# Kernel optimization log

Measured on AMD Instinct MI355X. Metric: run time of the kernel, lower is better.

Reference implementation:

```python
import jax, jax.numpy as jnp
import numpy as np

B, N, P, D, NH, DFFN = 4, 1024, 128, 512, 8, 2048
DH = D // NH  # 64


def setup_inputs() -> dict:
    key = jax.random.key(0)
    ks = jax.random.split(key, 64)
    i = [0]
    def rn(shape, s=1.0):
        k = ks[i[0]]; i[0] += 1
        return jax.random.normal(k, shape, jnp.float32) * s
    w = 0.05  # weight init scale
    inp = {
        "H": rn((B, N, D)),
        "V": rn((B, N, 3, D)),
        "D_batch": rn((B, N, N)),
        "rbf_bias": rn((B, 1, N, N)),  # rbf_feat_batch[layer_idx]
        "prompt_feature": rn((B * P, D)),
        # self-attn params
        "Wq": rn((4 * D, D), w), "bq": jnp.zeros((4 * D,), jnp.float32),
        "Wk": rn((4 * D, D), w), "bk": jnp.zeros((4 * D,), jnp.float32),
        "Wv": rn((D, D), w), "bv": jnp.zeros((D,), jnp.float32),
        "Wvv": rn((D, D), w),
        "Wo": rn((D, D), w), "bo": jnp.zeros((D,), jnp.float32),
        "Wvo": rn((D, D), w),
        "ln1_g": jnp.ones((D,), jnp.float32), "ln1_b": jnp.zeros((D,), jnp.float32),
        # cross-attn params (nn.MultiheadAttention packed in_proj + out_proj, then scaler_o)
        "ca_in_w": rn((3 * D, D), w), "ca_in_b": jnp.zeros((3 * D,), jnp.float32),
        "ca_out_w": rn((D, D), w), "ca_out_b": jnp.zeros((D,), jnp.float32),
        "ca_so_w": rn((D, D), w), "ca_so_b": jnp.zeros((D,), jnp.float32),
        "ln2_g": jnp.ones((D,), jnp.float32), "ln2_b": jnp.zeros((D,), jnp.float32),
        # GVP-FFN params
        "ffn_lv": rn((2 * D, D), w),
        "ffn_w1": rn((DFFN, 2 * D), w), "ffn_b1": jnp.zeros((DFFN,), jnp.float32),
        "ffn_w2": rn((2 * D, DFFN), w), "ffn_b2": jnp.zeros((2 * D,), jnp.float32),
        "ln3_g": jnp.ones((D,), jnp.float32), "ln3_b": jnp.zeros((D,), jnp.float32),
        # key-validity mask [B,N]
        "H_mask": jax.random.randint(ks[60], (B, N), 0, 2).astype(jnp.int32),
    }
    return inp


def _ln(x, g, b):
    m = x.mean(-1, keepdims=True)
    v = ((x - m) ** 2).mean(-1, keepdims=True)
    return (x - m) / jnp.sqrt(v + 1e-5) * g + b


def _ept_layer(H, V, D_batch, rbf_bias, prompt_feature,
               Wq, bq, Wk, bk, Wv, bv, Wvv, Wo, bo, Wvo, ln1_g, ln1_b,
               ca_in_w, ca_in_b, ca_out_w, ca_out_b, ca_so_w, ca_so_b, ln2_g, ln2_b,
               ffn_lv, ffn_w1, ffn_b1, ffn_w2, ffn_b2, ln3_g, ln3_b, H_mask):
    factor = 0.5 / np.sqrt(DH)
    # ---- self-attn sublayer (pre-LN on H, residual on H and V) ----
    H0, V0 = H, V
    Hn = _ln(H, ln1_g, ln1_b)
    Hq = (Hn @ Wq.T + bq).reshape(B, N, NH, 4 * DH)
    Hk = (Hn @ Wk.T + bk).reshape(B, N, NH, 4 * DH)
    Hv = (Hn @ Wv.T + bv).reshape(B, N, NH, DH)
    # vector values: [B,N,3,D] -> [B,N,3,NH,DH] -> [B,N,NH,3,DH] -> [B,N,NH,3*DH]
    Vv = (V @ Wvv.T).reshape(B, N, 3, NH, DH).transpose(0, 1, 3, 2, 4).reshape(B, N, NH, 3 * DH)
    V_attn = jnp.concatenate([Hv, Vv], axis=-1)  # [B,N,NH,4*DH]
    bias = rbf_bias + D_batch[:, None]           # [B,1,N,N]
    bias = jnp.where(H_mask[:, None, None, :] == 0, -jnp.inf, bias)
    scores = jnp.einsum('bnhd,bmhd->bhnm', Hq, Hk) * factor + bias
    attn = jax.nn.softmax(scores, axis=-1)
    res = jnp.einsum('bhnm,bmhd->bnhd', attn, V_attn)  # [B,N,NH,4*DH]
    H_res = res[..., :DH].reshape(B, N, D)
    V_res = res[..., DH:].reshape(B, N, NH, 3, DH).transpose(0, 1, 3, 2, 4).reshape(B, N, 3, D)
    H = (H_res @ Wo.T + bo) + H0
    V = (V_res @ Wvo.T) + V0
    # ---- cross-attn sublayer (pre-LN, residual on H only) ----
    H0 = H
    Hn = _ln(H, ln2_g, ln2_b)
    prompt = prompt_feature.reshape(B, P, D)
    Wq_c, Wk_c, Wv_c = ca_in_w[:D], ca_in_w[D:2 * D], ca_in_w[2 * D:]
    bq_c, bk_c, bv_c = ca_in_b[:D], ca_in_b[D:2 * D], ca_in_b[2 * D:]
    q = (Hn @ Wq_c.T + bq_c).reshape(B, N, NH, DH)
    k = (prompt @ Wk_c.T + bk_c).reshape(B, P, NH, DH)
    v = (prompt @ Wv_c.T + bv_c).reshape(B, P, NH, DH)
    ca = jax.nn.softmax(jnp.einsum('bnhd,bphd->bhnp', q, k) / np.sqrt(DH), axis=-1)
    co = jnp.einsum('bhnp,bphd->bnhd', ca, v).reshape(B, N, D)
    co = co @ ca_out_w.T + ca_out_b
    H = (co @ ca_so_w.T + ca_so_b) + H0
    # ---- GVP-FFN sublayer (pre-LN on H, residual on H and V) ----
    H0, V0 = H, V
    Hn = _ln(H, ln3_g, ln3_b)
    Vp = V @ ffn_lv.T                  # [B,N,3,2D]
    V1, V2 = Vp[..., :D], Vp[..., D:]
    scaler = jnp.concatenate([Hn, jnp.linalg.norm(V1, axis=-2)], axis=-1)  # [B,N,2D]
    h1 = jax.nn.silu(scaler @ ffn_w1.T + ffn_b1)
    so = h1 @ ffn_w2.T + ffn_b2        # [B,N,2D]
    H_out, V_upd = so[..., :D], so[..., D:]
    H = H_out + H0
    V = V_upd[..., None, :] * V2 + V0  # vector_act == 'none'
    return H, V


def reference(H, V, D_batch, rbf_bias, prompt_feature,
              Wq, bq, Wk, bk, Wv, bv, Wvv, Wo, bo, Wvo, ln1_g, ln1_b,
              ca_in_w, ca_in_b, ca_out_w, ca_out_b, ca_so_w, ca_so_b, ln2_g, ln2_b,
              ffn_lv, ffn_w1, ffn_b1, ffn_w2, ffn_b2, ln3_g, ln3_b, H_mask):
    return _ept_layer(H, V, D_batch, rbf_bias, prompt_feature,
                      Wq, bq, Wk, bk, Wv, bv, Wvv, Wo, bo, Wvo, ln1_g, ln1_b,
                      ca_in_w, ca_in_b, ca_out_w, ca_out_b, ca_so_w, ca_so_b, ln2_g, ln2_b,
                      ffn_lv, ffn_w1, ffn_b1, ffn_w2, ffn_b2, ln3_g, ln3_b, H_mask)
```

## Files before the change

kernel.cpp:

```cpp
#include <hip/hip_runtime.h>
#include <cstdint>
#include <cstddef>

#define B_    4
#define N_    1024
#define P_    128
#define D_    512
#define NH_   8

typedef unsigned short ushort_t;
typedef short short8 __attribute__((ext_vector_type(8)));
typedef float f32x4 __attribute__((ext_vector_type(4)));
typedef ushort_t ushort4_t __attribute__((ext_vector_type(4)));

__device__ inline ushort_t f2bf(float f) {
  union { float fp; unsigned int u; } v; v.fp = f;
  unsigned int r = v.u + 0x7fffu + ((v.u >> 16) & 1u);
  return (ushort_t)(r >> 16);
}
__device__ inline float bf2f(ushort_t u) {
  union { unsigned int i; float f; } v; v.i = ((unsigned int)u) << 16;
  return v.f;
}

__device__ __forceinline__ void gll16(const ushort_t* g, ushort_t* l) {
  __builtin_amdgcn_global_load_lds(
      (const __attribute__((address_space(1))) void*)g,
      (__attribute__((address_space(3))) void*)l, 16, 0, 0);
}

__device__ inline void cast8(const float* __restrict__ s, ushort_t* __restrict__ d,
                             unsigned i) {
  const float* sp = s + (size_t)i * 8;
  short8 o;
#pragma unroll
  for (int j = 0; j < 8; ++j) o[j] = (short)f2bf(sp[j]);
  *(short8*)(d + (size_t)i * 8) = o;
}

__global__ __launch_bounds__(256) void cast_fused(
    const float* s0, ushort_t* d0,  const float* s1, ushort_t* d1,
    const float* s2, ushort_t* d2,  const float* s3, ushort_t* d3,
    const float* s4, ushort_t* d4,  const float* s5, ushort_t* d5,
    const float* s6, ushort_t* d6,  const float* s7, ushort_t* d7,
    const float* s8, ushort_t* d8,  const float* s9, ushort_t* d9,
    const float* s10, ushort_t* d10, const float* s11, ushort_t* d11,
    const float* s12, ushort_t* d12, const float* s13, ushort_t* d13)
{
  unsigned i = blockIdx.x * 256 + threadIdx.x;
#define SEG(s, d, n8) if (i < (n8)) { cast8(s, d, i); return; } i -= (n8);
  SEG(s0, d0, 131072u)
  SEG(s1, d1, 131072u)
  SEG(s2, d2, 32768u)
  SEG(s3, d3, 32768u)
  SEG(s4, d4, 32768u)
  SEG(s5, d5, 32768u)
  SEG(s6, d6, 98304u)
  SEG(s7, d7, 32768u)
  SEG(s8, d8, 32768u)
  SEG(s9, d9, 65536u)
  SEG(s10, d10, 262144u)
  SEG(s11, d11, 262144u)
  SEG(s12, d12, 32768u)
  SEG(s13, d13, 786432u)
#undef SEG
}

__global__ __launch_bounds__(256) void biasmerge(const float* __restrict__ bq,
                                                 const float* __restrict__ bk,
                                                 float* __restrict__ o)
{
  int i = blockIdx.x * 256 + threadIdx.x;
  o[i] = (i < 2048) ? bq[i] : bk[i - 2048];
}

__global__ __launch_bounds__(256) void biascomb(const float* __restrict__ Db,
                                                const float* __restrict__ rbf,
                                                const int* __restrict__ mask,
                                                ushort_t* __restrict__ out)
{
  size_t i = (size_t)blockIdx.x * 256 + threadIdx.x;
  size_t e = i * 4;
  int b  = (int)(e >> 20);
  int m0 = (int)(e & 1023);
  float4 r = *(const float4*)(rbf + e);
  float4 d = *(const float4*)(Db + e);
  const int* mp = mask + b * 1024 + m0;
  ushort4_t o;
  o.x = f2bf(mp[0] ? r.x + d.x : -1e30f);
  o.y = f2bf(mp[1] ? r.y + d.y : -1e30f);
  o.z = f2bf(mp[2] ? r.z + d.z : -1e30f);
  o.w = f2bf(mp[3] ? r.w + d.w : -1e30f);
  *(ushort4_t*)(out + e) = o;
}

__global__ __launch_bounds__(256) void ln_kernel(
    const float* __restrict__ x, const float* __restrict__ g,
    const float* __restrict__ bb, ushort_t* __restrict__ y, int ostride)
{
  int row = blockIdx.x;
  int t = threadIdx.x;
  const float* xr = x + (size_t)row * D_;
  float a = xr[t], c = xr[t + 256];
  float s = a + c, sq = a * a + c * c;
#pragma unroll
  for (int off = 32; off >= 1; off >>= 1) {
    s  += __shfl_xor(s, off);
    sq += __shfl_xor(sq, off);
  }
  __shared__ float red[8];
  int w = t >> 6, lane = t & 63;
  if (lane == 0) { red[w] = s; red[4 + w] = sq; }
  __syncthreads();
  float st  = red[0] + red[1] + red[2] + red[3];
  float sqt = red[4] + red[5] + red[6] + red[7];
  float mean = st * (1.0f / D_);
  float var  = sqt * (1.0f / D_) - mean * mean;
  float inv  = rsqrtf(var + 1e-5f);
  y[(size_t)row * ostride + t]       = f2bf((a - mean) * inv * g[t] + bb[t]);
  y[(size_t)row * ostride + t + 256] = f2bf((c - mean) * inv * g[t + 256] + bb[t + 256]);
}

__global__ __launch_bounds__(256) void gemm_bf16(
    const ushort_t* __restrict__ A, const ushort_t* __restrict__ W,
    const float* __restrict__ bias, const float* __restrict__ res,
    float* __restrict__ Cf, ushort_t* __restrict__ Cb,
    int M, int N, int K, int flags)
{
  __shared__ __align__(16) ushort_t Al[128 * 32];
  __shared__ __align__(16) ushort_t Wl[128 * 32];
  const int t = threadIdx.x;
  const int wv = t >> 6, lane = t & 63, lr = lane & 15, lk = lane >> 4;
  const int wr = wv >> 1, wc = wv & 1;
  const size_t row0 = (size_t)blockIdx.y * 128;
  const size_t col0 = (size_t)blockIdx.x * 128;

  const int srow = 32 * wv + (lane >> 2);
  const int scol = (((lane & 3) ^ ((lane >> 3) & 3))) * 8;
  const ushort_t* ApG = A + (row0 + srow) * (size_t)K + scol;
  const ushort_t* WpG = W + (col0 + srow) * (size_t)K + scol;
  ushort_t* AlD = Al + (size_t)(32 * wv) * 32;
  ushort_t* WlD = Wl + (size_t)(32 * wv) * 32;
  const size_t K16 = (size_t)16 * K;

  f32x4 acc[4][4];
#pragma unroll
  for (int i = 0; i < 4; ++i)
#pragma unroll
    for (int j = 0; j < 4; ++j) acc[i][j] = f32x4{0.f, 0.f, 0.f, 0.f};

  const int sx = (lr >> 1) & 3;

  for (int k0 = 0; k0 < K; k0 += 32) {
    __syncthreads();
    gll16(ApG + k0,       AlD);
    gll16(ApG + k0 + K16, AlD + 512);
    gll16(WpG + k0,       WlD);
    gll16(WpG + k0 + K16, WlD + 512);
    __syncthreads();
    short8 af[4], bf[4];
#pragma unroll
    for (int i = 0; i < 4; ++i)
      af[i] = *(const short8*)&Al[(wr * 64 + i * 16 + lr) * 32 + ((lk ^ sx) << 3)];
#pragma unroll
    for (int j = 0; j < 4; ++j)
      bf[j] = *(const short8*)&Wl[(wc * 64 + j * 16 + lr) * 32 + ((lk ^ sx) << 3)];
#pragma unroll
    for (int i = 0; i < 4; ++i)
#pragma unroll
      for (int j = 0; j < 4; ++j)
        acc[i][j] = __builtin_amdgcn_mfma_f32_16x16x32_bf16(af[i], bf[j], acc[i][j], 0, 0, 0);
  }

  const int orow = wr * 64 + lk * 4, ocol = wc * 64 + lr;
#pragma unroll
  for (int i = 0; i < 4; ++i) {
#pragma unroll
    for (int j = 0; j < 4; ++j) {
      size_t colb = col0 + ocol + j * 16;
      float bv = (flags & 1) ? bias[colb] : 0.f;
#pragma unroll
      for (int r = 0; r < 4; ++r) {
        size_t rowg = row0 + orow + i * 16 + r;
        float v = acc[i][j][r] + bv;
        if (flags & 4) v = v / (1.f + __expf(-v));
        if (flags & 2) v += res[rowg * N + colb];
        if (flags & 8)  Cf[rowg * N + colb] = v;
        if (flags & 16) Cb[rowg * N + colb] = f2bf(v);
      }
    }
  }
}

__global__ __launch_bounds__(256) void vt_build(
    const ushort_t* __restrict__ HVb, const ushort_t* __restrict__ VVTb,
    ushort_t* __restrict__ VT)
{
  const int bh = blockIdx.z, b = bh >> 3, h = bh & 7;
  const int n0 = blockIdx.x * 64, dt = blockIdx.y;
  __shared__ __align__(16) ushort_t tile[64][72];
  const int t = threadIdx.x;
  {
    int r = t >> 2, c0 = (t & 3) * 16;
    const ushort_t* src = (dt == 0)
      ? HVb + ((size_t)(b * 1024 + n0 + r)) * 512 + h * 64 + c0
      : VVTb + (((size_t)(b * 1024 + n0 + r)) * 3 + (dt - 1)) * 512 + h * 64 + c0;
    *(short8*)&tile[r][c0]     = *(const short8*)src;
    *(short8*)&tile[r][c0 + 8] = *(const short8*)(src + 8);
  }
  __syncthreads();
  {
    int d = t >> 2, nc = (t & 3) * 16;
    short8 o0, o1;
#pragma unroll
    for (int i = 0; i < 8; ++i) { o0[i] = tile[nc + i][d]; o1[i] = tile[nc + 8 + i][d]; }
    ushort_t* dst = VT + ((size_t)bh * 256 + dt * 64 + d) * 1024 + n0 + nc;
    *(short8*)dst = o0;
    *(short8*)(dst + 8) = o1;
  }
}

__global__ __launch_bounds__(256) void attn_mfma(
    const ushort_t* __restrict__ QKg, const ushort_t* __restrict__ VTg,
    const ushort_t* __restrict__ biasb,
    ushort_t* __restrict__ HRESb, ushort_t* __restrict__ VRESb)
{
  const int bh = blockIdx.y, b = bh >> 3, h = bh & 7;
  const int q0 = blockIdx.x * 64;
  const int t = threadIdx.x, w = t >> 6, lane = t & 63, lr = lane & 15, lk = lane >> 4;

  __shared__ __align__(16) ushort_t Kl[32][264];
  __shared__ __align__(16) ushort_t Vl[256][40];
  __shared__ __align__(16) ushort_t Pl[4][16][40];

  short8 qf[8];
  {
    const ushort_t* qb = QKg + ((size_t)(b * 1024 + q0 + w * 16 + lr)) * 4096 + h * 256;
#pragma unroll
    for (int s = 0; s < 8; ++s) qf[s] = *(const short8*)(qb + s * 32 + lk * 8);
  }
  f32x4 o[16];
#pragma unroll
  for (int i = 0; i < 16; ++i) o[i] = f32x4{0.f, 0.f, 0.f, 0.f};
  float mrow[4] = {-1e30f, -1e30f, -1e30f, -1e30f};
  float lsum[4] = {0.f, 0.f, 0.f, 0.f};
  const int qrow = q0 + w * 16 + lk * 4;

  const int krow = t >> 3, kc = (t & 7) * 32;
  const ushort_t* ksrc = QKg + ((size_t)(b * 1024 + krow)) * 4096 + 2048 + h * 256 + kc;
  const ushort_t* vsrc = VTg + ((size_t)bh * 256 + t) * 1024;
  const int vrot = (t >> 3) & 3;

  for (int k0 = 0; k0 < 1024; k0 += 32) {
    __syncthreads();
    {
      const ushort_t* ks = ksrc + (size_t)k0 * 4096;
#pragma unroll
      for (int c = 0; c < 4; ++c)
        *(short8*)&Kl[krow][kc + c * 8] = *(const short8*)(ks + c * 8);
#pragma unroll
      for (int c = 0; c < 4; ++c) {
        int cc = (c + vrot) & 3;
        *(short8*)&Vl[t][cc * 8] = *(const short8*)(vsrc + k0 + cc * 8);
      }
    }
    __syncthreads();

    f32x4 s2[2];
    s2[0] = f32x4{0.f, 0.f, 0.f, 0.f};
    s2[1] = f32x4{0.f, 0.f, 0.f, 0.f};
    __builtin_amdgcn_s_setprio(1);
#pragma unroll
    for (int ks = 0; ks < 8; ++ks) {
#pragma unroll
      for (int j = 0; j < 2; ++j) {
        short8 kf = *(const short8*)&Kl[j * 16 + lr][ks * 32 + lk * 8];
        s2[j] = __builtin_amdgcn_mfma_f32_16x16x32_bf16(qf[ks], kf, s2[j], 0, 0, 0);
      }
    }
    __builtin_amdgcn_s_setprio(0);

    float sv[2][4];
    const ushort_t* bp = biasb + ((size_t)b << 20) + (size_t)qrow * 1024 + k0 + lr;
#pragma unroll
    for (int r = 0; r < 4; ++r) {
      sv[0][r] = s2[0][r] * 0.0625f + bf2f(bp[r * 1024]);
      sv[1][r] = s2[1][r] * 0.0625f + bf2f(bp[r * 1024 + 16]);
    }
    float pm[4], need = -1e30f;
#pragma unroll
    for (int r = 0; r < 4; ++r) {
      float m2 = fmaxf(sv[0][r], sv[1][r]);
      m2 = fmaxf(m2, __shfl_xor(m2, 1));
      m2 = fmaxf(m2, __shfl_xor(m2, 2));
      m2 = fmaxf(m2, __shfl_xor(m2, 4));
      m2 = fmaxf(m2, __shfl_xor(m2, 8));
      pm[r] = m2;
      need = fmaxf(need, m2 - mrow[r]);
    }
    if (!__all(need <= 8.f)) {
#pragma unroll
      for (int r = 0; r < 4; ++r) {
        float mn = fmaxf(mrow[r], pm[r]);
        float al = __expf(mrow[r] - mn);
        mrow[r] = mn;
        lsum[r] *= al;
#pragma unroll
        for (int d = 0; d < 16; ++d) o[d][r] *= al;
      }
    }
#pragma unroll
    for (int r = 0; r < 4; ++r) {
      float p0 = __expf(sv[0][r] - mrow[r]);
      float p1 = __expf(sv[1][r] - mrow[r]);
      float rs = p0 + p1;
      rs += __shfl_xor(rs, 1); rs += __shfl_xor(rs, 2);
      rs += __shfl_xor(rs, 4); rs += __shfl_xor(rs, 8);
      lsum[r] += rs;
      Pl[w][lk * 4 + r][lr]      = f2bf(p0);
      Pl[w][lk * 4 + r][16 + lr] = f2bf(p1);
    }
    short8 pf = *(const short8*)&Pl[w][lr][lk * 8];
    __builtin_amdgcn_s_setprio(1);
#pragma unroll
    for (int d = 0; d < 16; ++d) {
      short8 vf = *(const short8*)&Vl[d * 16 + lr][lk * 8];
      o[d] = __builtin_amdgcn_mfma_f32_16x16x32_bf16(pf, vf, o[d], 0, 0, 0);
    }
    __builtin_amdgcn_s_setprio(0);
  }

  float inv[4];
#pragma unroll
  for (int r = 0; r < 4; ++r) inv[r] = 1.f / lsum[r];
#pragma unroll
  for (int d = 0; d < 16; ++d) {
    int dcat = d * 16 + lr;
#pragma unroll
    for (int r = 0; r < 4; ++r) {
      float v = o[d][r] * inv[r];
      int n = qrow + r;
      if (dcat < 64)
        HRESb[((size_t)b * 1024 + n) * 512 + h * 64 + dcat] = f2bf(v);
      else {
        int c = (dcat - 64) >> 6, jj = (dcat - 64) & 63;
        VRESb[(((size_t)b * 1024 + n) * 3 + c) * 512 + h * 64 + jj] = f2bf(v);
      }
    }
  }
}

__global__ __launch_bounds__(256) void attn_cross_mfma(
    const ushort_t* __restrict__ Qb, const ushort_t* __restrict__ KVb,
    ushort_t* __restrict__ COb)
{
  const int bh = blockIdx.y, b = bh >> 3, h = bh & 7;
  const int q0 = blockIdx.x * 64;
  const int t = threadIdx.x, w = t >> 6, lane = t & 63, lr = lane & 15, lk = lane >> 4;

  __shared__ __align__(16) ushort_t Kl[128][72];
  __shared__ __align__(16) ushort_t Vt[64][136];
  __shared__ __align__(16) ushort_t Pl[4][16][136];

  {
    int p = t >> 1, c0 = (t & 1) * 32;
    const ushort_t* kp = KVb + ((size_t)b * 128 + p) * 1024 + h * 64 + c0;
#pragma unroll
    for (int i = 0; i < 4; ++i) {
      short8 kv = *(const short8*)(kp + i * 8);
      *(short8*)&Kl[p][c0 + i * 8] = kv;
      short8 vv = *(const short8*)(kp + 512 + i * 8);
#pragma unroll
      for (int jj = 0; jj < 8; ++jj) Vt[c0 + i * 8 + jj][p] = (ushort_t)vv[jj];
    }
  }
  __syncthreads();

  short8 qf[2];
  {
    const ushort_t* qp = Qb + ((size_t)b * 1024 + q0 + w * 16 + lr) * 512 + h * 64;
    qf[0] = *(const short8*)(qp + lk * 8);
    qf[1] = *(const short8*)(qp + 32 + lk * 8);
  }

  f32x4 s[8];
#pragma unroll
  for (int j = 0; j < 8; ++j) s[j] = f32x4{0.f, 0.f, 0.f, 0.f};
#pragma unroll
  for (int ks = 0; ks < 2; ++ks)
#pragma unroll
    for (int j = 0; j < 8; ++j) {
      short8 kf = *(const short8*)&Kl[j * 16 + lr][ks * 32 + lk * 8];
      s[j] = __builtin_amdgcn_mfma_f32_16x16x32_bf16(qf[ks], kf, s[j], 0, 0, 0);
    }

  float linv[4];
#pragma unroll
  for (int r = 0; r < 4; ++r) {
    float sc[8];
#pragma unroll
    for (int j = 0; j < 8; ++j) sc[j] = s[j][r] * 0.125f;
    float mx = sc[0];
#pragma unroll
    for (int j = 1; j < 8; ++j) mx = fmaxf(mx, sc[j]);
    mx = fmaxf(mx, __shfl_xor(mx, 1));
    mx = fmaxf(mx, __shfl_xor(mx, 2));
    mx = fmaxf(mx, __shfl_xor(mx, 4));
    mx = fmaxf(mx, __shfl_xor(mx, 8));
    float rs = 0.f;
#pragma unroll
    for (int j = 0; j < 8; ++j) {
      float p = __expf(sc[j] - mx);
      rs += p;
      Pl[w][lk * 4 + r][j * 16 + lr] = f2bf(p);
    }
    rs += __shfl_xor(rs, 1); rs += __shfl_xor(rs, 2);
    rs += __shfl_xor(rs, 4); rs += __shfl_xor(rs, 8);
    linv[r] = 1.f / rs;
  }
  __syncthreads();

  f32x4 o[4];
#pragma unroll
  for (int d = 0; d < 4; ++d) o[d] = f32x4{0.f, 0.f, 0.f, 0.f};
#pragma unroll
  for (int ks = 0; ks < 4; ++ks) {
    short8 pf = *(const short8*)&Pl[w][lr][ks * 32 + lk * 8];
#pragma unroll
    for (int d = 0; d < 4; ++d) {
      short8 vf = *(const short8*)&Vt[d * 16 + lr][ks * 32 + lk * 8];
      o[d] = __builtin_amdgcn_mfma_f32_16x16x32_bf16(pf, vf, o[d], 0, 0, 0);
    }
  }

#pragma unroll
  for (int d = 0; d < 4; ++d)
#pragma unroll
    for (int r = 0; r < 4; ++r) {
      int n = q0 + w * 16 + lk * 4 + r;
      COb[((size_t)b * 1024 + n) * 512 + h * 64 + d * 16 + lr] = f2bf(o[d][r] * linv[r]);
    }
}

__global__ __launch_bounds__(256) void vnorm_kernel(
    const ushort_t* __restrict__ Vp, ushort_t* __restrict__ scal)
{
  size_t i = (size_t)blockIdx.x * 256 + threadIdx.x;
  size_t bn = i >> 9; int d = (int)(i & 511);
  size_t base = bn * 3 * 1024 + d;
  float a = bf2f(Vp[base]);
  float b = bf2f(Vp[base + 1024]);
  float c = bf2f(Vp[base + 2048]);
  scal[bn * 1024 + 512 + d] = f2bf(sqrtf(a * a + b * b + c * c));
}

__global__ __launch_bounds__(256) void final_kernel(
    const float* __restrict__ so, const float* __restrict__ H2,
    const ushort_t* __restrict__ Vp, const float* __restrict__ Vnew,
    float* __restrict__ out)
{
  size_t i = (size_t)blockIdx.x * 256 + threadIdx.x;
  size_t bn = i >> 9; int d = (int)(i & 511);
  out[bn * 512 + d] = so[bn * 1024 + d] + H2[bn * 512 + d];
  float vu = so[bn * 1024 + 512 + d];
  float* outV = out + (size_t)B_ * N_ * D_;
#pragma unroll
  for (int c = 0; c < 3; ++c) {
    size_t vi = (bn * 3 + c) * 512 + d;
    outV[vi] = vu * bf2f(Vp[(bn * 3 + c) * 1024 + 512 + d]) + Vnew[vi];
  }
}

extern "C" void kernel_launch(void* const* d_in, const int* in_sizes, int n_in,
                              void* d_out, int out_size, void* d_ws, size_t ws_size,
                              hipStream_t stream)
{
  const float* H      = (const float*)d_in[0];
  const float* V      = (const float*)d_in[1];
  const float* Db     = (const float*)d_in[2];
  const float* rbf    = (const float*)d_in[3];
  const float* prompt = (const float*)d_in[4];
  const float* Wq  = (const float*)d_in[5];
  const float* bq  = (const float*)d_in[6];
  const float* Wk  = (const float*)d_in[7];
  const float* bk  = (const float*)d_in[8];
  const float* Wv  = (const float*)d_in[9];
  const float* bv  = (const float*)d_in[10];
  const float* Wvv = (const float*)d_in[11];
  const float* Wo  = (const float*)d_in[12];
  const float* bo  = (const float*)d_in[13];
  const float* Wvo = (const float*)d_in[14];
  const float* ln1g = (const float*)d_in[15];
  const float* ln1b = (const float*)d_in[16];
  const float* caw  = (const float*)d_in[17];
  const float* cab  = (const float*)d_in[18];
  const float* caow = (const float*)d_in[19];
  const float* caob = (const float*)d_in[20];
  const float* casw = (const float*)d_in[21];
  const float* casb = (const float*)d_in[22];
  const float* ln2g = (const float*)d_in[23];
  const float* ln2b = (const float*)d_in[24];
  const float* flv  = (const float*)d_in[25];
  const float* fw1  = (const float*)d_in[26];
  const float* fb1  = (const float*)d_in[27];
  const float* fw2  = (const float*)d_in[28];
  const float* fb2  = (const float*)d_in[29];
  const float* ln3g = (const float*)d_in[30];
  const float* ln3b = (const float*)d_in[31];
  const int*   mask = (const int*)d_in[32];

  char* wsb = (char*)d_ws;
  float* out = (float*)d_out;

#define HMB(x) ((size_t)(x) << 19)
  ushort_t* Wqkb  = (ushort_t*)(wsb + HMB(0));
  ushort_t* Wvb   = (ushort_t*)(wsb + HMB(8));
  ushort_t* Wvvb  = (ushort_t*)(wsb + HMB(9));
  ushort_t* Wob   = (ushort_t*)(wsb + HMB(10));
  ushort_t* Wvob  = (ushort_t*)(wsb + HMB(11));
  ushort_t* cawb  = (ushort_t*)(wsb + HMB(12));
  ushort_t* caowb = (ushort_t*)(wsb + HMB(15));
  ushort_t* caswb = (ushort_t*)(wsb + HMB(16));
  ushort_t* flvb  = (ushort_t*)(wsb + HMB(17));
  ushort_t* fw1b  = (ushort_t*)(wsb + HMB(19));
  ushort_t* fw2b  = (ushort_t*)(wsb + HMB(27));
  ushort_t* promptb = (ushort_t*)(wsb + HMB(35));
  float*    BQK   = (float*)   (wsb + HMB(36));
  ushort_t* HQKb  = (ushort_t*)(wsb + HMB(37));
  float*    VNEW  = (float*)   (wsb + HMB(37));
  float*    H2    = (float*)   (wsb + HMB(85));
  ushort_t* HNb   = (ushort_t*)(wsb + HMB(101));
  ushort_t* VT    = (ushort_t*)(wsb + HMB(101));
  ushort_t* QCb   = (ushort_t*)(wsb + HMB(101));
  ushort_t* KVCb  = (ushort_t*)(wsb + HMB(109));
  ushort_t* SCALb = (ushort_t*)(wsb + HMB(101));
  ushort_t* Vb    = (ushort_t*)(wsb + HMB(133));
  ushort_t* HRESb = (ushort_t*)(wsb + HMB(133));
  ushort_t* HN2b  = (ushort_t*)(wsb + HMB(133));
  ushort_t* VPb   = (ushort_t*)(wsb + HMB(133));
  ushort_t* VRESb = (ushort_t*)(wsb + HMB(141));
  ushort_t* COb   = (ushort_t*)(wsb + HMB(141));
  ushort_t* CO2b  = (ushort_t*)(wsb + HMB(149));
  ushort_t* HVb   = (ushort_t*)(wsb + HMB(157));
  ushort_t* VVTb  = (ushort_t*)(wsb + HMB(165));
  float*    H1    = (float*)   (wsb + HMB(165));
  ushort_t* BIASCb= (ushort_t*)(wsb + HMB(189));
  float*    SO    = (float*)   (wsb + HMB(189));
  ushort_t* VNEWb = (ushort_t*)(wsb + HMB(221));
  ushort_t* HH1b  = (ushort_t*)(wsb + HMB(245));

  cast_fused<<<7680, 256, 0, stream>>>(
      Wq, Wqkb, Wk, Wqkb + (size_t)2048 * 512, Wv, Wvb, Wvv, Wvvb, Wo, Wob,
      Wvo, Wvob, caw, cawb, caow, caowb, casw, caswb, flv, flvb,
      fw1, fw1b, fw2, fw2b, prompt, promptb, V, Vb);
  biasmerge<<<16, 256, 0, stream>>>(bq, bk, BQK);
  biascomb<<<4096, 256, 0, stream>>>(Db, rbf, mask, BIASCb);
  ln_kernel<<<4096, 256, 0, stream>>>(H, ln1g, ln1b, HNb, 512);

  gemm_bf16<<<dim3(32, 32), 256, 0, stream>>>(HNb, Wqkb, BQK, nullptr, nullptr, HQKb, 4096, 4096, 512, 1 | 16);
  gemm_bf16<<<dim3(4, 32), 256, 0, stream>>>(HNb, Wvb, bv, nullptr, nullptr, HVb, 4096, 512, 512, 1 | 16);
  gemm_bf16<<<dim3(4, 96), 256, 0, stream>>>(Vb, Wvvb, nullptr, nullptr, nullptr, VVTb, 12288, 512, 512, 16);

  vt_build<<<dim3(16, 4, 32), 256, 0, stream>>>(HVb, VVTb, VT);

  attn_mfma<<<dim3(16, 32), 256, 0, stream>>>(HQKb, VT, BIASCb, HRESb, VRESb);

  gemm_bf16<<<dim3(4, 32), 256, 0, stream>>>(HRESb, Wob, bo, H, H1, nullptr, 4096, 512, 512, 1 | 2 | 8);
  gemm_bf16<<<dim3(4, 96), 256, 0, stream>>>(VRESb, Wvob, nullptr, V, VNEW, VNEWb, 12288, 512, 512, 2 | 8 | 16);

  ln_kernel<<<4096, 256, 0, stream>>>(H1, ln2g, ln2b, HN2b, 512);
  gemm_bf16<<<dim3(4, 32), 256, 0, stream>>>(HN2b, cawb, cab, nullptr, nullptr, QCb, 4096, 512, 512, 1 | 16);
  gemm_bf16<<<dim3(8, 4), 256, 0, stream>>>(promptb, cawb + 262144, cab + 512, nullptr, nullptr, KVCb, 512, 1024, 512, 1 | 16);

  attn_cross_mfma<<<dim3(16, 32), 256, 0, stream>>>(QCb, KVCb, COb);

  gemm_bf16<<<dim3(4, 32), 256, 0, stream>>>(COb, caowb, caob, nullptr, nullptr, CO2b, 4096, 512, 512, 1 | 16);
  gemm_bf16<<<dim3(4, 32), 256, 0, stream>>>(CO2b, caswb, casb, H1, H2, nullptr, 4096, 512, 512, 1 | 2 | 8);

  gemm_bf16<<<dim3(8, 96), 256, 0, stream>>>(VNEWb, flvb, nullptr, nullptr, nullptr, VPb, 12288, 1024, 512, 16);
  ln_kernel<<<4096, 256, 0, stream>>>(H2, ln3g, ln3b, SCALb, 1024);
  vnorm_kernel<<<8192, 256, 0, stream>>>(VPb, SCALb);

  gemm_bf16<<<dim3(16, 32), 256, 0, stream>>>(SCALb, fw1b, fb1, nullptr, nullptr, HH1b, 4096, 2048, 1024, 1 | 4 | 16);
  gemm_bf16<<<dim3(8, 32), 256, 0, stream>>>(HH1b, fw2b, fb2, nullptr, SO, nullptr, 4096, 1024, 2048, 1 | 8);

  final_kernel<<<8192, 256, 0, stream>>>(SO, H2, VPb, VNEW, out);

  (void)in_sizes; (void)n_in; (void)out_size; (void)ws_size;
}
```

Measured before the change: 550.3 us.

## Prefetch K/V tiles into registers, swizzle K LDS, remap blocks per XCD

The attention kernel now loads the next K and V tile into registers while the current tile is being computed, hiding global-load latency behind the MFMA work. The K shared-memory tile drops its padding and uses an XOR swizzle to avoid bank conflicts. Both the GEMM and attention kernels remap their block indices so that blocks sharing data land on the same XCD, improving L2 reuse on the chiplet layout. The trade-off is higher register pressure from the prefetch buffers, and the remap assumes the block count divides by 8.

```diff
diff --git a/kernel.cpp b/kernel.cpp
--- a/kernel.cpp
+++ b/kernel.cpp
@@ -132,8 +132,13 @@
   const int t = threadIdx.x;
   const int wv = t >> 6, lane = t & 63, lr = lane & 15, lk = lane >> 4;
   const int wr = wv >> 1, wc = wv & 1;
-  const size_t row0 = (size_t)blockIdx.y * 128;
-  const size_t col0 = (size_t)blockIdx.x * 128;
+
+  const int gx = gridDim.x;
+  const int lid = blockIdx.y * gx + blockIdx.x;
+  const int cpx = (gx * gridDim.y) >> 3;
+  const int nlid = (lid & 7) * cpx + (lid >> 3);
+  const size_t row0 = (size_t)(nlid / gx) * 128;
+  const size_t col0 = (size_t)(nlid % gx) * 128;
 
   const int srow = 32 * wv + (lane >> 2);
   const int scol = (((lane & 3) ^ ((lane >> 3) & 3))) * 8;
@@ -225,11 +230,13 @@
     const ushort_t* __restrict__ biasb,
     ushort_t* __restrict__ HRESb, ushort_t* __restrict__ VRESb)
 {
-  const int bh = blockIdx.y, b = bh >> 3, h = bh & 7;
-  const int q0 = blockIdx.x * 64;
+  const int blk = blockIdx.x;
+  const int bi = blk >> 3;
+  const int bh = (blk & 7) * 4 + (bi >> 4), b = bh >> 3, h = bh & 7;
+  const int q0 = (bi & 15) * 64;
   const int t = threadIdx.x, w = t >> 6, lane = t & 63, lr = lane & 15, lk = lane >> 4;
 
-  __shared__ __align__(16) ushort_t Kl[32][264];
+  __shared__ __align__(16) ushort_t Kl[32 * 256];
   __shared__ __align__(16) ushort_t Vl[256][40];
   __shared__ __align__(16) ushort_t Pl[4][16][40];
 
@@ -246,25 +253,43 @@
   float lsum[4] = {0.f, 0.f, 0.f, 0.f};
   const int qrow = q0 + w * 16 + lk * 4;
 
-  const int krow = t >> 3, kc = (t & 7) * 32;
-  const ushort_t* ksrc = QKg + ((size_t)(b * 1024 + krow)) * 4096 + 2048 + h * 256 + kc;
+  const int krow = w * 8 + (lane & 7);
+  const int kcb  = (lane >> 3) * 32;
+  const ushort_t* ksrc = QKg + ((size_t)(b * 1024 + krow)) * 4096 + 2048 + h * 256 + kcb;
   const ushort_t* vsrc = VTg + ((size_t)bh * 256 + t) * 1024;
   const int vrot = (t >> 3) & 3;
+  const int kswz = (krow & 7) << 3;
+
+  short8 kreg[4], vreg[4];
+#define LOADT(k0_) do {                                                        \
+    const ushort_t* ks_ = ksrc + (size_t)(k0_) * 4096;                         \
+    kreg[0] = *(const short8*)(ks_);                                           \
+    kreg[1] = *(const short8*)(ks_ + 8);                                       \
+    kreg[2] = *(const short8*)(ks_ + 16);                                      \
+    kreg[3] = *(const short8*)(ks_ + 24);                                      \
+    _Pragma("unroll")                                                          \
+    for (int c_ = 0; c_ < 4; ++c_) {                                           \
+      int cc_ = (c_ + vrot) & 3;                                               \
+      vreg[c_] = *(const short8*)(vsrc + (k0_) + cc_ * 8);                     \
+    }                                                                          \
+  } while (0)
+
+  LOADT(0);
 
   for (int k0 = 0; k0 < 1024; k0 += 32) {
     __syncthreads();
     {
-      const ushort_t* ks = ksrc + (size_t)k0 * 4096;
 #pragma unroll
       for (int c = 0; c < 4; ++c)
-        *(short8*)&Kl[krow][kc + c * 8] = *(const short8*)(ks + c * 8);
+        *(short8*)&Kl[(krow * 256 + kcb + c * 8) ^ kswz] = kreg[c];
 #pragma unroll
       for (int c = 0; c < 4; ++c) {
         int cc = (c + vrot) & 3;
-        *(short8*)&Vl[t][cc * 8] = *(const short8*)(vsrc + k0 + cc * 8);
+        *(short8*)&Vl[t][cc * 8] = vreg[c];
       }
     }
     __syncthreads();
+    if (k0 + 32 < 1024) LOADT(k0 + 32);
 
     f32x4 s2[2];
     s2[0] = f32x4{0.f, 0.f, 0.f, 0.f};
@@ -274,7 +299,8 @@
     for (int ks = 0; ks < 8; ++ks) {
 #pragma unroll
       for (int j = 0; j < 2; ++j) {
-        short8 kf = *(const short8*)&Kl[j * 16 + lr][ks * 32 + lk * 8];
+        int row = j * 16 + lr;
+        short8 kf = *(const short8*)&Kl[(row * 256 + ks * 32 + lk * 8) ^ ((row & 7) << 3)];
         s2[j] = __builtin_amdgcn_mfma_f32_16x16x32_bf16(qf[ks], kf, s2[j], 0, 0, 0);
       }
     }
@@ -329,6 +355,7 @@
     }
     __builtin_amdgcn_s_setprio(0);
   }
+#undef LOADT
 
   float inv[4];
 #pragma unroll
@@ -563,7 +590,7 @@
 
   vt_build<<<dim3(16, 4, 32), 256, 0, stream>>>(HVb, VVTb, VT);
 
-  attn_mfma<<<dim3(16, 32), 256, 0, stream>>>(HQKb, VT, BIASCb, HRESb, VRESb);
+  attn_mfma<<<512, 256, 0, stream>>>(HQKb, VT, BIASCb, HRESb, VRESb);
 
   gemm_bf16<<<dim3(4, 32), 256, 0, stream>>>(HRESb, Wob, bo, H, H1, nullptr, 4096, 512, 512, 1 | 2 | 8);
   gemm_bf16<<<dim3(4, 96), 256, 0, stream>>>(VRESb, Wvob, nullptr, V, VNEW, VNEWb, 12288, 512, 512, 2 | 8 | 16);
```

Result: slower. 607.8 us (+10.4%).

## Add 64-row GEMM variant, XCD-aware block remap, and retile small GEMMs

Applied to the files above, without the earlier changes.

Adds gemm_bf16_sm, a GEMM variant with a 64x128 tile, and switches the small 4096x512 and 512x1024 GEMMs, plus the FFN second GEMM, to it so more workgroups fill the GPU. Both GEMM kernels now remap the linear block id so that consecutive tiles are grouped per XCD (stride by 8), aiming for better L2 locality. The K-tile load thread mapping in attn_mfma is also changed. The smaller tiles lower per-block arithmetic intensity and raise operand reload traffic. The remap assumes the block count is divisible by 8.

```diff
diff --git a/kernel.cpp b/kernel.cpp
--- a/kernel.cpp
+++ b/kernel.cpp
@@ -132,8 +132,13 @@
   const int t = threadIdx.x;
   const int wv = t >> 6, lane = t & 63, lr = lane & 15, lk = lane >> 4;
   const int wr = wv >> 1, wc = wv & 1;
-  const size_t row0 = (size_t)blockIdx.y * 128;
-  const size_t col0 = (size_t)blockIdx.x * 128;
+
+  const int gx = gridDim.x;
+  const int lid = blockIdx.y * gx + blockIdx.x;
+  const int cpx = (gx * gridDim.y) >> 3;
+  const int nlid = (lid & 7) * cpx + (lid >> 3);
+  const size_t row0 = (size_t)(nlid / gx) * 128;
+  const size_t col0 = (size_t)(nlid % gx) * 128;
 
   const int srow = 32 * wv + (lane >> 2);
   const int scol = (((lane & 3) ^ ((lane >> 3) & 3))) * 8;
@@ -175,6 +180,82 @@
   const int orow = wr * 64 + lk * 4, ocol = wc * 64 + lr;
 #pragma unroll
   for (int i = 0; i < 4; ++i) {
+#pragma unroll
+    for (int j = 0; j < 4; ++j) {
+      size_t colb = col0 + ocol + j * 16;
+      float bv = (flags & 1) ? bias[colb] : 0.f;
+#pragma unroll
+      for (int r = 0; r < 4; ++r) {
+        size_t rowg = row0 + orow + i * 16 + r;
+        float v = acc[i][j][r] + bv;
+        if (flags & 4) v = v / (1.f + __expf(-v));
+        if (flags & 2) v += res[rowg * N + colb];
+        if (flags & 8)  Cf[rowg * N + colb] = v;
+        if (flags & 16) Cb[rowg * N + colb] = f2bf(v);
+      }
+    }
+  }
+}
+
+__global__ __launch_bounds__(256) void gemm_bf16_sm(
+    const ushort_t* __restrict__ A, const ushort_t* __restrict__ W,
+    const float* __restrict__ bias, const float* __restrict__ res,
+    float* __restrict__ Cf, ushort_t* __restrict__ Cb,
+    int M, int N, int K, int flags)
+{
+  __shared__ __align__(16) ushort_t Al[64 * 32];
+  __shared__ __align__(16) ushort_t Wl[128 * 32];
+  const int t = threadIdx.x;
+  const int wv = t >> 6, lane = t & 63, lr = lane & 15, lk = lane >> 4;
+  const int wr = wv >> 1, wc = wv & 1;
+
+  const int gx = gridDim.x;
+  const int lid = blockIdx.y * gx + blockIdx.x;
+  const int cpx = (gx * gridDim.y) >> 3;
+  const int nlid = (lid & 7) * cpx + (lid >> 3);
+  const size_t row0 = (size_t)(nlid / gx) * 64;
+  const size_t col0 = (size_t)(nlid % gx) * 128;
+
+  const int scol = (((lane & 3) ^ ((lane >> 3) & 3))) * 8;
+  const int srowA = 16 * wv + (lane >> 2);
+  const int srowW = 32 * wv + (lane >> 2);
+  const ushort_t* ApG = A + (row0 + srowA) * (size_t)K + scol;
+  const ushort_t* WpG = W + (col0 + srowW) * (size_t)K + scol;
+  ushort_t* AlD = Al + (size_t)(16 * wv) * 32;
+  ushort_t* WlD = Wl + (size_t)(32 * wv) * 32;
+  const size_t K16 = (size_t)16 * K;
+
+  f32x4 acc[2][4];
+#pragma unroll
+  for (int i = 0; i < 2; ++i)
+#pragma unroll
+    for (int j = 0; j < 4; ++j) acc[i][j] = f32x4{0.f, 0.f, 0.f, 0.f};
+
+  const int sx = (lr >> 1) & 3;
+
+  for (int k0 = 0; k0 < K; k0 += 32) {
+    __syncthreads();
+    gll16(ApG + k0,       AlD);
+    gll16(WpG + k0,       WlD);
+    gll16(WpG + k0 + K16, WlD + 512);
+    __syncthreads();
+    short8 af[2], bf[4];
+#pragma unroll
+    for (int i = 0; i < 2; ++i)
+      af[i] = *(const short8*)&Al[(wr * 32 + i * 16 + lr) * 32 + ((lk ^ sx) << 3)];
+#pragma unroll
+    for (int j = 0; j < 4; ++j)
+      bf[j] = *(const short8*)&Wl[(wc * 64 + j * 16 + lr) * 32 + ((lk ^ sx) << 3)];
+#pragma unroll
+    for (int i = 0; i < 2; ++i)
+#pragma unroll
+      for (int j = 0; j < 4; ++j)
+        acc[i][j] = __builtin_amdgcn_mfma_f32_16x16x32_bf16(af[i], bf[j], acc[i][j], 0, 0, 0);
+  }
+
+  const int orow = wr * 32 + lk * 4, ocol = wc * 64 + lr;
+#pragma unroll
+  for (int i = 0; i < 2; ++i) {
 #pragma unroll
     for (int j = 0; j < 4; ++j) {
       size_t colb = col0 + ocol + j * 16;
@@ -246,7 +327,8 @@
   float lsum[4] = {0.f, 0.f, 0.f, 0.f};
   const int qrow = q0 + w * 16 + lk * 4;
 
-  const int krow = t >> 3, kc = (t & 7) * 32;
+  const int krow = w * 8 + (lane & 7);
+  const int kc   = (lane >> 3) * 32;
   const ushort_t* ksrc = QKg + ((size_t)(b * 1024 + krow)) * 4096 + 2048 + h * 256 + kc;
   const ushort_t* vsrc = VTg + ((size_t)bh * 256 + t) * 1024;
   const int vrot = (t >> 3) & 3;
@@ -558,31 +640,31 @@
   ln_kernel<<<4096, 256, 0, stream>>>(H, ln1g, ln1b, HNb, 512);
 
   gemm_bf16<<<dim3(32, 32), 256, 0, stream>>>(HNb, Wqkb, BQK, nullptr, nullptr, HQKb, 4096, 4096, 512, 1 | 16);
-  gemm_bf16<<<dim3(4, 32), 256, 0, stream>>>(HNb, Wvb, bv, nullptr, nullptr, HVb, 4096, 512, 512, 1 | 16);
+  gemm_bf16_sm<<<dim3(4, 64), 256, 0, stream>>>(HNb, Wvb, bv, nullptr, nullptr, HVb, 4096, 512, 512, 1 | 16);
   gemm_bf16<<<dim3(4, 96), 256, 0, stream>>>(Vb, Wvvb, nullptr, nullptr, nullptr, VVTb, 12288, 512, 512, 16);
 
   vt_build<<<dim3(16, 4, 32), 256, 0, stream>>>(HVb, VVTb, VT);
 
   attn_mfma<<<dim3(16, 32), 256, 0, stream>>>(HQKb, VT, BIASCb, HRESb, VRESb);
 
-  gemm_bf16<<<dim3(4, 32), 256, 0, stream>>>(HRESb, Wob, bo, H, H1, nullptr, 4096, 512, 512, 1 | 2 | 8);
+  gemm_bf16_sm<<<dim3(4, 64), 256, 0, stream>>>(HRESb, Wob, bo, H, H1, nullptr, 4096, 512, 512, 1 | 2 | 8);
   gemm_bf16<<<dim3(4, 96), 256, 0, stream>>>(VRESb, Wvob, nullptr, V, VNEW, VNEWb, 12288, 512, 512, 2 | 8 | 16);
 
   ln_kernel<<<4096, 256, 0, stream>>>(H1, ln2g, ln2b, HN2b, 512);
-  gemm_bf16<<<dim3(4, 32), 256, 0, stream>>>(HN2b, cawb, cab, nullptr, nullptr, QCb, 4096, 512, 512, 1 | 16);
-  gemm_bf16<<<dim3(8, 4), 256, 0, stream>>>(promptb, cawb + 262144, cab + 512, nullptr, nullptr, KVCb, 512, 1024, 512, 1 | 16);
+  gemm_bf16_sm<<<dim3(4, 64), 256, 0, stream>>>(HN2b, cawb, cab, nullptr, nullptr, QCb, 4096, 512, 512, 1 | 16);
+  gemm_bf16_sm<<<dim3(8, 8), 256, 0, stream>>>(promptb, cawb + 262144, cab + 512, nullptr, nullptr, KVCb, 512, 1024, 512, 1 | 16);
 
   attn_cross_mfma<<<dim3(16, 32), 256, 0, stream>>>(QCb, KVCb, COb);
 
-  gemm_bf16<<<dim3(4, 32), 256, 0, stream>>>(COb, caowb, caob, nullptr, nullptr, CO2b, 4096, 512, 512, 1 | 16);
-  gemm_bf16<<<dim3(4, 32), 256, 0, stream>>>(CO2b, caswb, casb, H1, H2, nullptr, 4096, 512, 512, 1 | 2 | 8);
+  gemm_bf16_sm<<<dim3(4, 64), 256, 0, stream>>>(COb, caowb, caob, nullptr, nullptr, CO2b, 4096, 512, 512, 1 | 16);
+  gemm_bf16_sm<<<dim3(4, 64), 256, 0, stream>>>(CO2b, caswb, casb, H1, H2, nullptr, 4096, 512, 512, 1 | 2 | 8);
 
   gemm_bf16<<<dim3(8, 96), 256, 0, stream>>>(VNEWb, flvb, nullptr, nullptr, nullptr, VPb, 12288, 1024, 512, 16);
   ln_kernel<<<4096, 256, 0, stream>>>(H2, ln3g, ln3b, SCALb, 1024);
   vnorm_kernel<<<8192, 256, 0, stream>>>(VPb, SCALb);
 
   gemm_bf16<<<dim3(16, 32), 256, 0, stream>>>(SCALb, fw1b, fb1, nullptr, nullptr, HH1b, 4096, 2048, 1024, 1 | 4 | 16);
-  gemm_bf16<<<dim3(8, 32), 256, 0, stream>>>(HH1b, fw2b, fb2, nullptr, SO, nullptr, 4096, 1024, 2048, 1 | 8);
+  gemm_bf16_sm<<<dim3(8, 64), 256, 0, stream>>>(HH1b, fw2b, fb2, nullptr, SO, nullptr, 4096, 1024, 2048, 1 | 8);
 
   final_kernel<<<8192, 256, 0, stream>>>(SO, H2, VPb, VNEW, out);
 
```

Result: faster. 491.8 us (-10.6%).
